# Performance work log

Hardware: AMD Instinct MI355X
Metric: run time of the kernel (lower is better)

## Reference

```python
import jax, jax.numpy as jnp
import numpy as np

D_MODEL = 1024
NUM_HEADS = 16
D_K = D_MODEL // NUM_HEADS


def setup_inputs() -> dict:
    key = jax.random.key(0)
    ks = jax.random.split(key, 9)
    s = 1.0 / np.sqrt(D_MODEL)
    x = jax.random.normal(ks[0], (2, 2048, D_MODEL), dtype=jnp.float32)
    mk = lambda k: jax.random.uniform(k, (D_MODEL, D_MODEL), jnp.float32, -s, s)
    mb = lambda k: jax.random.uniform(k, (D_MODEL,), jnp.float32, -s, s)
    return {
        "x": x,
        "Wq": mk(ks[1]), "bq": mb(ks[2]),
        "Wk": mk(ks[3]), "bk": mb(ks[4]),
        "Wv": mk(ks[5]), "bv": mb(ks[6]),
        "Wo": mk(ks[7]), "bo": mb(ks[8]),
    }


def _attn(x, Wq, bq, Wk, bk, Wv, bv, Wo, bo):
    B, S, _ = x.shape
    # torch Linear: y = x @ W.T + b; weights stored [out, in]
    def proj(W, b):
        y = jnp.einsum('bsd,ed->bse', x, W) + b
        return y.reshape(B, S, NUM_HEADS, D_K).transpose(0, 2, 1, 3)  # [B,H,S,Dk]
    Q = proj(Wq, bq)
    K = proj(Wk, bk)
    V = proj(Wv, bv)
    scale = 1.0 / np.sqrt(D_K).astype(np.float32)
    scores = jnp.einsum('bhqd,bhkd->bhqk', Q, K) * scale  # [B,H,S,S]
    # FAITHFUL to source: softmax over dim=1 (the HEAD axis), a quirk of the original code
    attn = jax.nn.softmax(scores, axis=1)
    context = jnp.einsum('bhqk,bhkd->bhqd', attn, V)  # [B,H,S,Dk]
    context = context.transpose(0, 2, 1, 3).reshape(B, S, D_MODEL)
    return jnp.einsum('bsd,ed->bse', context, Wo) + bo


def reference(x, Wq, bq, Wk, bk, Wv, bv, Wo, bo):
    return _attn(x, Wq, bq, Wk, bk, Wv, bv, Wo, bo)
```

## Files before the change

kernel.cpp:

```cpp
#include <hip/hip_runtime.h>


#define D_MODEL 1024
#define NH 16
#define DKH 64
#define SEQ 2048
#define NB 2
#define NTOK (NB * SEQ)

typedef float f32x4 __attribute__((ext_vector_type(4)));
typedef short bf16x8 __attribute__((ext_vector_type(8)));

static __device__ __forceinline__ unsigned short f2bf(float x) {
    union { float f; unsigned int u; } c; c.f = x;
    unsigned int r = (c.u + 0x7FFFu + ((c.u >> 16) & 1u)) >> 16;
    return (unsigned short)r;
}
static __device__ __forceinline__ unsigned int pack2(float a, float b) {
    return (unsigned int)f2bf(a) | ((unsigned int)f2bf(b) << 16);
}
static __device__ __forceinline__ unsigned int pack2rn(float a, float b) {
    union { float f; unsigned int u; } ca, cb; ca.f = a; cb.f = b;
    return __builtin_amdgcn_perm(cb.u + 0x8000u, ca.u + 0x8000u, 0x07060302u);
}
static __device__ __forceinline__ float bflo(unsigned int u) {
    union { unsigned int x; float f; } c; c.x = u << 16; return c.f;
}
static __device__ __forceinline__ float bfhi(unsigned int u) {
    union { unsigned int x; float f; } c; c.x = u & 0xFFFF0000u; return c.f;
}
static __device__ __forceinline__ f32x4 mfma16(uint4 a, uint4 b, f32x4 c) {
    return __builtin_amdgcn_mfma_f32_16x16x32_bf16(
        __builtin_bit_cast(bf16x8, a), __builtin_bit_cast(bf16x8, b), c, 0, 0, 0);
}
static __device__ __forceinline__ void gl_lds16(const unsigned short* g, unsigned short* l) {
    __builtin_amdgcn_global_load_lds(
        (const __attribute__((address_space(1))) unsigned int*)g,
        (__attribute__((address_space(3))) unsigned int*)l, 16, 0, 0);
}
static __device__ __forceinline__ int fsw(int row) {
    return (row & 7) ^ ((row >> 2) & 7);
}

__global__ __launch_bounds__(256) void cvt_k(const float* __restrict__ x,
                                             unsigned short* __restrict__ xb)
{
    size_t i = ((size_t)blockIdx.x * 256 + threadIdx.x) * 8;
    float4 a = *(const float4*)(x + i);
    float4 b = *(const float4*)(x + i + 4);
    uint4 p = { pack2(a.x, a.y), pack2(a.z, a.w), pack2(b.x, b.y), pack2(b.z, b.w) };
    *(uint4*)(xb + i) = p;
}

__global__ __launch_bounds__(256) void cvt_w3(
    const float* __restrict__ w0, const float* __restrict__ w1,
    const float* __restrict__ w2, unsigned short* __restrict__ outb)
{
    int sel = blockIdx.x >> 9;
    int blk = blockIdx.x & 511;
    const float* src = (sel == 0) ? w0 : (sel == 1) ? w1 : w2;
    size_t i = ((size_t)blk * 256 + threadIdx.x) * 8;
    float4 a = *(const float4*)(src + i);
    float4 b = *(const float4*)(src + i + 4);
    uint4 p = { pack2(a.x, a.y), pack2(a.z, a.w), pack2(b.x, b.y), pack2(b.z, b.w) };
    *(uint4*)(outb + (size_t)sel * D_MODEL * D_MODEL + i) = p;
}

__global__ __launch_bounds__(256) void gemm_qkv3(
    const unsigned short* __restrict__ A, const unsigned short* __restrict__ Wb3,
    const float* __restrict__ bq, const float* __restrict__ bk,
    const float* __restrict__ bv, unsigned short* __restrict__ Qh,
    unsigned short* __restrict__ Kh, unsigned short* __restrict__ Vt)
{
    __shared__ unsigned short lds[16384];
    unsigned short* lA = lds;
    unsigned short* lB = lds + 8192;
    const int tid = threadIdx.x;
    const int wv = tid >> 6, lane = tid & 63, quad = lane >> 4, lm = lane & 15;
    const int sel = blockIdx.x >> 3;
    const int m0 = blockIdx.y * 128, n0 = (blockIdx.x & 7) * 128;
    const int sub = lane >> 3, chl = (lane & 7) ^ sub;
    const unsigned short* Wb = Wb3 + (size_t)sel * D_MODEL * D_MODEL;
    const float* bias = (sel == 0) ? bq : (sel == 1) ? bk : bv;
    const float osc = (sel == 0) ? 0.125f : 1.0f;

    f32x4 acc[2][8] = {};

    for (int k0 = 0; k0 < D_MODEL; k0 += 64) {
        __syncthreads();
#pragma unroll
        for (int j = 0; j < 4; ++j) {
            int rbase = wv * 32 + j * 8;
            gl_lds16(A + (size_t)(m0 + rbase + sub) * D_MODEL + k0 + chl * 8,
                     &lA[rbase * 64]);
            gl_lds16(Wb + (size_t)(n0 + rbase + sub) * D_MODEL + k0 + chl * 8,
                     &lB[rbase * 64]);
        }
        __syncthreads();
#pragma unroll
        for (int ks = 0; ks < 2; ++ks) {
            uint4 af[2];
#pragma unroll
            for (int mt = 0; mt < 2; ++mt)
                af[mt] = *(const uint4*)&lA[(wv * 32 + mt * 16 + lm) * 64 +
                                            ((ks * 4 + quad) ^ (lm & 7)) * 8];
#pragma unroll
            for (int nt = 0; nt < 8; ++nt) {
                uint4 bf = *(const uint4*)&lB[(nt * 16 + lm) * 64 +
                                              ((ks * 4 + quad) ^ (lm & 7)) * 8];
                acc[0][nt] = mfma16(af[0], bf, acc[0][nt]);
                acc[1][nt] = mfma16(af[1], bf, acc[1][nt]);
            }
        }
    }

    if (sel < 2) {
        unsigned short* out = (sel == 0) ? Qh : Kh;
#pragma unroll
        for (int nt = 0; nt < 8; ++nt) {
            int n = n0 + nt * 16 + lm;
            float bvv = bias[n];
            int h = n >> 6, d = n & 63;
#pragma unroll
            for (int mt = 0; mt < 2; ++mt)
#pragma unroll
                for (int r = 0; r < 4; ++r) {
                    int m = m0 + wv * 32 + mt * 16 + quad * 4 + r;
                    int b = m >> 11, q = m & 2047;
                    out[((size_t)(b * NH + h) * SEQ + q) * DKH + d] =
                        f2bf((acc[mt][nt][r] + bvv) * osc);
                }
        }
    } else {
        __syncthreads();
        unsigned short* T = lds;
#pragma unroll
        for (int nt = 0; nt < 8; ++nt) {
            float bvv = bias[n0 + nt * 16 + lm];
            int nl = nt * 16 + lm;
#pragma unroll
            for (int mt = 0; mt < 2; ++mt) {
                int ml = wv * 32 + mt * 16 + quad * 4;
                uint2 p = { pack2rn(acc[mt][nt][0] + bvv, acc[mt][nt][1] + bvv),
                            pack2rn(acc[mt][nt][2] + bvv, acc[mt][nt][3] + bvv) };
                *(uint2*)&T[nl * 128 + ml] = p;
            }
        }
        __syncthreads();
        int row = tid >> 1, seg = tid & 1;
        int b = m0 >> 11, s0 = m0 & 2047;
        unsigned short* dst = Vt + ((size_t)(b * D_MODEL) + n0 + row) * SEQ + s0 + seg * 64;
        const unsigned short* src = &T[row * 128 + seg * 64];
#pragma unroll
        for (int i = 0; i < 8; ++i)
            *(uint4*)(dst + i * 8) = *(const uint4*)(src + i * 8);
    }
}

template <int KS>
__global__ __launch_bounds__(256) void psum(const unsigned short* __restrict__ OP,
                                            unsigned short* __restrict__ OPs)
{
    const size_t M = (size_t)NTOK * D_MODEL;
    size_t i = ((size_t)blockIdx.x * 256 + threadIdx.x) * 8;
    uint4 a = *(const uint4*)(OP + i);
    float lo0 = bflo(a.x), hi0 = bfhi(a.x), lo1 = bflo(a.y), hi1 = bfhi(a.y);
    float lo2 = bflo(a.z), hi2 = bfhi(a.z), lo3 = bflo(a.w), hi3 = bfhi(a.w);
#pragma unroll
    for (int p = 1; p < KS; ++p) {
        uint4 u = *(const uint4*)(OP + p * M + i);
        lo0 += bflo(u.x); hi0 += bfhi(u.x); lo1 += bflo(u.y); hi1 += bfhi(u.y);
        lo2 += bflo(u.z); hi2 += bfhi(u.z); lo3 += bflo(u.w); hi3 += bfhi(u.w);
    }
    uint4 o = { pack2(lo0, hi0), pack2(lo1, hi1), pack2(lo2, hi2), pack2(lo3, hi3) };
    *(uint4*)(OPs + i) = o;
}

__global__ __launch_bounds__(256) void gemm_osum1(
    const unsigned short* __restrict__ OPs, const unsigned short* __restrict__ WoB,
    const float* __restrict__ bias, float* __restrict__ out)
{
    __shared__ unsigned short lds[16384];
    unsigned short* lA = lds;
    unsigned short* lB = lds + 8192;
    const int tid = threadIdx.x;
    const int wv = tid >> 6, lane = tid & 63, quad = lane >> 4, lm = lane & 15;
    const int m0 = blockIdx.y * 128, n0 = blockIdx.x * 128;
    const int sub = lane >> 3, chl = (lane & 7) ^ sub;
    const int b = m0 >> 11, q0 = m0 & 2047;

    f32x4 acc[2][8] = {};

    for (int k0 = 0; k0 < D_MODEL; k0 += 64) {
        const int h = k0 >> 6;
        const unsigned short* Ab = OPs + ((size_t)(b * NH + h) * SEQ + q0) * DKH;
        __syncthreads();
#pragma unroll
        for (int j = 0; j < 4; ++j) {
            int rbase = wv * 32 + j * 8;
            gl_lds16(Ab + (size_t)(rbase + sub) * DKH + chl * 8, &lA[rbase * 64]);
            gl_lds16(WoB + (size_t)(n0 + rbase + sub) * D_MODEL + k0 + chl * 8,
                     &lB[rbase * 64]);
        }
        __syncthreads();
#pragma unroll
        for (int ks = 0; ks < 2; ++ks) {
            uint4 af[2];
#pragma unroll
            for (int mt = 0; mt < 2; ++mt)
                af[mt] = *(const uint4*)&lA[(wv * 32 + mt * 16 + lm) * 64 +
                                            ((ks * 4 + quad) ^ (lm & 7)) * 8];
#pragma unroll
            for (int nt = 0; nt < 8; ++nt) {
                uint4 bf = *(const uint4*)&lB[(nt * 16 + lm) * 64 +
                                              ((ks * 4 + quad) ^ (lm & 7)) * 8];
                acc[0][nt] = mfma16(af[0], bf, acc[0][nt]);
                acc[1][nt] = mfma16(af[1], bf, acc[1][nt]);
            }
        }
    }
#pragma unroll
    for (int nt = 0; nt < 8; ++nt) {
        int n = n0 + nt * 16 + lm;
        float bv = bias[n];
#pragma unroll
        for (int mt = 0; mt < 2; ++mt)
#pragma unroll
            for (int r = 0; r < 4; ++r) {
                int m = m0 + wv * 32 + mt * 16 + quad * 4 + r;
                out[(size_t)m * D_MODEL + n] = acc[mt][nt][r] + bv;
            }
    }
}

__global__ __launch_bounds__(256) void zker2(
    const unsigned short* __restrict__ Qh, const unsigned short* __restrict__ Kh,
    unsigned short* __restrict__ rz)
{
    __shared__ unsigned short lK[128 * 64];
    const int tid = threadIdx.x;
    const int wv = tid >> 6, lane = tid & 63, quad = lane >> 4, lm = lane & 15;
    const int q0 = blockIdx.x * 128, k0 = blockIdx.y * 128, b = blockIdx.z;
    const int srow = tid >> 3, sc = tid & 7;

    f32x4 z[2][8] = {};

    for (int h = 0; h < NH; ++h) {
        const size_t kb = ((size_t)(b * NH + h) * SEQ + k0) * DKH;
        __syncthreads();
#pragma unroll
        for (int j = 0; j < 4; ++j) {
            int row = j * 32 + srow;
            int g = sc ^ fsw(row);
            gl_lds16(Kh + kb + (size_t)row * 64 + g * 8, &lK[(j * 32 + wv * 8) * 64]);
        }
        uint4 bq[2][2];
#pragma unroll
        for (int qs = 0; qs < 2; ++qs) {
            const unsigned short* qp = Qh +
                ((size_t)(b * NH + h) * SEQ + q0 + wv * 32 + qs * 16 + lm) * DKH + quad * 8;
            bq[qs][0] = *(const uint4*)qp;
            bq[qs][1] = *(const uint4*)(qp + 32);
        }
        __syncthreads();
#pragma unroll
        for (int kt = 0; kt < 8; ++kt) {
            int krow = kt * 16 + lm;
            uint4 a0 = *(const uint4*)&lK[krow * 64 + ((quad) ^ fsw(krow)) * 8];
            uint4 a1 = *(const uint4*)&lK[krow * 64 + ((4 + quad) ^ fsw(krow)) * 8];
#pragma unroll
            for (int qs = 0; qs < 2; ++qs) {
                f32x4 sf = {0.f, 0.f, 0.f, 0.f};
                sf = mfma16(a0, bq[qs][0], sf);
                sf = mfma16(a1, bq[qs][1], sf);
#pragma unroll
                for (int r = 0; r < 4; ++r)
                    z[qs][kt][r] += __expf(sf[r]);
            }
        }
    }
#pragma unroll
    for (int qs = 0; qs < 2; ++qs) {
        int q = q0 + wv * 32 + qs * 16 + lm;
#pragma unroll
        for (int kt = 0; kt < 8; ++kt) {
            int k = k0 + kt * 16 + quad * 4;
            uint2 st = { pack2rn(1.0f / z[qs][kt][0], 1.0f / z[qs][kt][1]),
                         pack2rn(1.0f / z[qs][kt][2], 1.0f / z[qs][kt][3]) };
            *(uint2*)(rz + (size_t)(b * SEQ + q) * SEQ + k) = st;
        }
    }
}

template <int KS>
__global__ __launch_bounds__(256) void attn4(
    const unsigned short* __restrict__ Qh, const unsigned short* __restrict__ Kh,
    const unsigned short* __restrict__ Vt, const unsigned short* __restrict__ rz,
    unsigned short* __restrict__ OP)
{
    __shared__ unsigned short lK[64 * 64];
    __shared__ unsigned short lV[64 * 64];
    const int tid = threadIdx.x;
    const int wv = tid >> 6, lane = tid & 63, quad = lane >> 4, lm = lane & 15;
    const int q0 = blockIdx.x * 128;
    const int bh = blockIdx.y, b = bh >> 4, h = bh & 15;
    const int ksl = blockIdx.z;
    const int NIT = (SEQ / KS) / 64;
    const int kbeg = ksl * (SEQ / KS);
    const int q0w = q0 + wv * 32;
    const size_t hb = (size_t)(b * NH + h) * SEQ;
    const int srow = tid >> 3, sc = tid & 7;

    uint4 qf[2][2];
#pragma unroll
    for (int qs = 0; qs < 2; ++qs)
#pragma unroll
        for (int ks = 0; ks < 2; ++ks)
            qf[qs][ks] = *(const uint4*)(Qh + (hb + q0w + qs * 16 + lm) * DKH +
                                         ks * 32 + quad * 8);

    const int perm = ((lm >> 2) * 8) + (lm & 3);
    f32x4 oa[4][2] = {};

    for (int kt = 0; kt < NIT; ++kt) {
        const int kbase = kbeg + kt * 64;
        __syncthreads();
#pragma unroll
        for (int j = 0; j < 2; ++j) {
            int row = j * 32 + srow;
            int g = sc ^ fsw(row);
            gl_lds16(Kh + (hb + kbase + row) * DKH + g * 8,
                     &lK[(j * 32 + wv * 8) * 64]);
        }
#pragma unroll
        for (int j = 0; j < 2; ++j) {
            int row = j * 32 + srow;
            int g = sc ^ fsw(row);
            gl_lds16(Vt + ((size_t)(b * D_MODEL) + h * DKH + row) * SEQ + kbase + g * 8,
                     &lV[(j * 32 + wv * 8) * 64]);
        }
        uint4 rv[2][2];
#pragma unroll
        for (int qs = 0; qs < 2; ++qs)
#pragma unroll
            for (int gr = 0; gr < 2; ++gr)
                rv[gr][qs] = *(const uint4*)(rz +
                    (size_t)(b * SEQ + q0w + qs * 16 + lm) * SEQ +
                    kbase + gr * 32 + quad * 8);
        __syncthreads();

#pragma unroll
        for (int gr = 0; gr < 2; ++gr) {
            f32x4 sf[2][2] = {};
#pragma unroll
            for (int sel = 0; sel < 2; ++sel) {
                int key = gr * 32 + perm + sel * 4;
#pragma unroll
                for (int ks = 0; ks < 2; ++ks) {
                    uint4 kfv = *(const uint4*)&lK[key * 64 +
                                                   ((ks * 4 + quad) ^ fsw(key)) * 8];
                    sf[sel][0] = mfma16(kfv, qf[0][ks], sf[sel][0]);
                    sf[sel][1] = mfma16(kfv, qf[1][ks], sf[sel][1]);
                }
            }
            uint4 pk[2];
#pragma unroll
            for (int qs = 0; qs < 2; ++qs) {
                uint4 rq = rv[gr][qs];
                float p00 = __expf(sf[0][qs][0]) * bflo(rq.x);
                float p01 = __expf(sf[0][qs][1]) * bfhi(rq.x);
                float p02 = __expf(sf[0][qs][2]) * bflo(rq.y);
                float p03 = __expf(sf[0][qs][3]) * bfhi(rq.y);
                float p10 = __expf(sf[1][qs][0]) * bflo(rq.z);
                float p11 = __expf(sf[1][qs][1]) * bfhi(rq.z);
                float p12 = __expf(sf[1][qs][2]) * bflo(rq.w);
                float p13 = __expf(sf[1][qs][3]) * bfhi(rq.w);
                pk[qs].x = pack2rn(p00, p01);
                pk[qs].y = pack2rn(p02, p03);
                pk[qs].z = pack2rn(p10, p11);
                pk[qs].w = pack2rn(p12, p13);
            }
#pragma unroll
            for (int ct = 0; ct < 4; ++ct) {
                int vrow = ct * 16 + lm;
                uint4 vfv = *(const uint4*)&lV[vrow * 64 +
                                               ((gr * 4 + quad) ^ fsw(vrow)) * 8];
                oa[ct][0] = mfma16(vfv, pk[0], oa[ct][0]);
                oa[ct][1] = mfma16(vfv, pk[1], oa[ct][1]);
            }
        }
    }

    unsigned short* op = OP + (size_t)ksl * NTOK * D_MODEL;
#pragma unroll
    for (int ct = 0; ct < 4; ++ct)
#pragma unroll
        for (int qs = 0; qs < 2; ++qs) {
            uint2 st = { pack2rn(oa[ct][qs][0], oa[ct][qs][1]),
                         pack2rn(oa[ct][qs][2], oa[ct][qs][3]) };
            *(uint2*)(op + (hb + q0w + qs * 16 + lm) * DKH + ct * 16 + quad * 4) = st;
        }
}

extern "C" void kernel_launch(void* const* d_in, const int* in_sizes, int n_in,
                              void* d_out, int out_size, void* d_ws, size_t ws_size,
                              hipStream_t stream)
{
    const float* x  = (const float*)d_in[0];
    const float* Wq = (const float*)d_in[1];
    const float* bq = (const float*)d_in[2];
    const float* Wk = (const float*)d_in[3];
    const float* bk = (const float*)d_in[4];
    const float* Wv = (const float*)d_in[5];
    const float* bv = (const float*)d_in[6];
    const float* Wo = (const float*)d_in[7];
    const float* bo = (const float*)d_in[8];
    float* out = (float*)d_out;

    const size_t M  = (size_t)NTOK * D_MODEL;
    const size_t RZ = (size_t)NB * SEQ * SEQ;
    unsigned short* ws = (unsigned short*)d_ws;
    unsigned short* rzb = ws;
    unsigned short* xb  = ws;
    unsigned short* Qh  = ws + RZ;
    unsigned short* Kh  = Qh + M;
    unsigned short* Vt  = Kh + M;
    unsigned short* OP  = Vt + M;
    unsigned short* Wb3 = OP;
    unsigned short* OPs = Qh;
    unsigned short* WoB = rzb;

    const size_t need4 = (RZ + 3 * M + 4 * M) * sizeof(unsigned short);
    const size_t need2 = (RZ + 3 * M + 2 * M) * sizeof(unsigned short);
    const int KS = (ws_size >= need4) ? 4 : (ws_size >= need2) ? 2 : 1;

    cvt_k<<<2048, 256, 0, stream>>>(x, xb);
    cvt_w3<<<1536, 256, 0, stream>>>(Wq, Wk, Wv, Wb3);
    gemm_qkv3<<<dim3(24, 32), 256, 0, stream>>>(xb, Wb3, bq, bk, bv, Qh, Kh, Vt);
    zker2<<<dim3(16, 16, NB), 256, 0, stream>>>(Qh, Kh, rzb);
    if (KS == 4)      attn4<4><<<dim3(16, NB * NH, 4), 256, 0, stream>>>(Qh, Kh, Vt, rzb, OP);
    else if (KS == 2) attn4<2><<<dim3(16, NB * NH, 2), 256, 0, stream>>>(Qh, Kh, Vt, rzb, OP);
    else              attn4<1><<<dim3(16, NB * NH, 1), 256, 0, stream>>>(Qh, Kh, Vt, rzb, OP);
    cvt_k<<<512, 256, 0, stream>>>(Wo, WoB);
    if (KS == 4)      psum<4><<<2048, 256, 0, stream>>>(OP, OPs);
    else if (KS == 2) psum<2><<<2048, 256, 0, stream>>>(OP, OPs);
    else              OPs = OP;
    gemm_osum1<<<dim3(8, 32), 256, 0, stream>>>(OPs, WoB, bo, out);
}
```

Measured before the change: 276.8 us.

## Use exp2 with folded log2e scale, store log-normalizer, remap blocks per XCD

The Q projection scale now includes log2(e), so scores come out in base 2 and the hardware exp2 can be used. The per-(q,k) normalizer is stored as a negative log2 sum and fed in as the MFMA accumulator's initial value, which folds the normalization into the score and removes a multiply per element. P is packed by truncation instead of round-to-nearest. Both attention kernels also get a 1D grid with a mapping that keeps tiles sharing K/V and rz data on the same XCD for L2 locality. The costs are a bf16-rounded log normalizer and truncated P values, which lose some precision.

```diff
diff --git a/kernel.cpp b/kernel.cpp
--- a/kernel.cpp
+++ b/kernel.cpp
@@ -7,6 +7,7 @@
 #define SEQ 2048
 #define NB 2
 #define NTOK (NB * SEQ)
+#define OSC 0.180336880f
 
 typedef float f32x4 __attribute__((ext_vector_type(4)));
 typedef short bf16x8 __attribute__((ext_vector_type(8)));
@@ -22,6 +23,10 @@
 static __device__ __forceinline__ unsigned int pack2rn(float a, float b) {
     union { float f; unsigned int u; } ca, cb; ca.f = a; cb.f = b;
     return __builtin_amdgcn_perm(cb.u + 0x8000u, ca.u + 0x8000u, 0x07060302u);
+}
+static __device__ __forceinline__ unsigned int pack2tr(float a, float b) {
+    union { float f; unsigned int u; } ca, cb; ca.f = a; cb.f = b;
+    return __builtin_amdgcn_perm(cb.u, ca.u, 0x07060302u);
 }
 static __device__ __forceinline__ float bflo(unsigned int u) {
     union { unsigned int x; float f; } c; c.x = u << 16; return c.f;
@@ -82,7 +87,7 @@
     const int sub = lane >> 3, chl = (lane & 7) ^ sub;
     const unsigned short* Wb = Wb3 + (size_t)sel * D_MODEL * D_MODEL;
     const float* bias = (sel == 0) ? bq : (sel == 1) ? bk : bv;
-    const float osc = (sel == 0) ? 0.125f : 1.0f;
+    const float osc = (sel == 0) ? OSC : 1.0f;
 
     f32x4 acc[2][8] = {};
 
@@ -240,19 +245,23 @@
     __shared__ unsigned short lK[128 * 64];
     const int tid = threadIdx.x;
     const int wv = tid >> 6, lane = tid & 63, quad = lane >> 4, lm = lane & 15;
-    const int q0 = blockIdx.x * 128, k0 = blockIdx.y * 128, b = blockIdx.z;
+    const int lid = blockIdx.x;
+    const int xcd = lid & 7, slot = lid >> 3;
+    const int qb = slot & 15, col = xcd * 4 + (slot >> 4);
+    const int b = col >> 4, kb = col & 15;
+    const int q0 = qb * 128, k0 = kb * 128;
     const int srow = tid >> 3, sc = tid & 7;
 
     f32x4 z[2][8] = {};
 
     for (int h = 0; h < NH; ++h) {
-        const size_t kb = ((size_t)(b * NH + h) * SEQ + k0) * DKH;
+        const size_t kbase = ((size_t)(b * NH + h) * SEQ + k0) * DKH;
         __syncthreads();
 #pragma unroll
         for (int j = 0; j < 4; ++j) {
             int row = j * 32 + srow;
             int g = sc ^ fsw(row);
-            gl_lds16(Kh + kb + (size_t)row * 64 + g * 8, &lK[(j * 32 + wv * 8) * 64]);
+            gl_lds16(Kh + kbase + (size_t)row * 64 + g * 8, &lK[(j * 32 + wv * 8) * 64]);
         }
         uint4 bq[2][2];
 #pragma unroll
@@ -275,7 +284,7 @@
                 sf = mfma16(a1, bq[qs][1], sf);
 #pragma unroll
                 for (int r = 0; r < 4; ++r)
-                    z[qs][kt][r] += __expf(sf[r]);
+                    z[qs][kt][r] += __builtin_amdgcn_exp2f(sf[r]);
             }
         }
     }
@@ -285,8 +294,11 @@
 #pragma unroll
         for (int kt = 0; kt < 8; ++kt) {
             int k = k0 + kt * 16 + quad * 4;
-            uint2 st = { pack2rn(1.0f / z[qs][kt][0], 1.0f / z[qs][kt][1]),
-                         pack2rn(1.0f / z[qs][kt][2], 1.0f / z[qs][kt][3]) };
+            float l0 = __builtin_amdgcn_logf(z[qs][kt][0]);
+            float l1 = __builtin_amdgcn_logf(z[qs][kt][1]);
+            float l2 = __builtin_amdgcn_logf(z[qs][kt][2]);
+            float l3 = __builtin_amdgcn_logf(z[qs][kt][3]);
+            uint2 st = { pack2rn(-l0, -l1), pack2rn(-l2, -l3) };
             *(uint2*)(rz + (size_t)(b * SEQ + q) * SEQ + k) = st;
         }
     }
@@ -302,9 +314,13 @@
     __shared__ unsigned short lV[64 * 64];
     const int tid = threadIdx.x;
     const int wv = tid >> 6, lane = tid & 63, quad = lane >> 4, lm = lane & 15;
-    const int q0 = blockIdx.x * 128;
-    const int bh = blockIdx.y, b = bh >> 4, h = bh & 15;
-    const int ksl = blockIdx.z;
+    const int lid = blockIdx.x;
+    const int xcd = lid & 7, slot = lid >> 3;
+    const int qb = slot & 15;
+    const int combo = xcd * (4 * KS) + (slot >> 4);
+    const int bh = combo / KS, ksl = combo % KS;
+    const int b = bh >> 4, h = bh & 15;
+    const int q0 = qb * 128;
     const int NIT = (SEQ / KS) / 64;
     const int kbeg = ksl * (SEQ / KS);
     const int q0w = q0 + wv * 32;
@@ -351,7 +367,15 @@
 
 #pragma unroll
         for (int gr = 0; gr < 2; ++gr) {
-            f32x4 sf[2][2] = {};
+            f32x4 sf[2][2];
+#pragma unroll
+            for (int qs = 0; qs < 2; ++qs) {
+                uint4 rq = rv[gr][qs];
+                sf[0][qs][0] = bflo(rq.x); sf[0][qs][1] = bfhi(rq.x);
+                sf[0][qs][2] = bflo(rq.y); sf[0][qs][3] = bfhi(rq.y);
+                sf[1][qs][0] = bflo(rq.z); sf[1][qs][1] = bfhi(rq.z);
+                sf[1][qs][2] = bflo(rq.w); sf[1][qs][3] = bfhi(rq.w);
+            }
 #pragma unroll
             for (int sel = 0; sel < 2; ++sel) {
                 int key = gr * 32 + perm + sel * 4;
@@ -366,19 +390,18 @@
             uint4 pk[2];
 #pragma unroll
             for (int qs = 0; qs < 2; ++qs) {
-                uint4 rq = rv[gr][qs];
-                float p00 = __expf(sf[0][qs][0]) * bflo(rq.x);
-                float p01 = __expf(sf[0][qs][1]) * bfhi(rq.x);
-                float p02 = __expf(sf[0][qs][2]) * bflo(rq.y);
-                float p03 = __expf(sf[0][qs][3]) * bfhi(rq.y);
-                float p10 = __expf(sf[1][qs][0]) * bflo(rq.z);
-                float p11 = __expf(sf[1][qs][1]) * bfhi(rq.z);
-                float p12 = __expf(sf[1][qs][2]) * bflo(rq.w);
-                float p13 = __expf(sf[1][qs][3]) * bfhi(rq.w);
-                pk[qs].x = pack2rn(p00, p01);
-                pk[qs].y = pack2rn(p02, p03);
-                pk[qs].z = pack2rn(p10, p11);
-                pk[qs].w = pack2rn(p12, p13);
+                float p00 = __builtin_amdgcn_exp2f(sf[0][qs][0]);
+                float p01 = __builtin_amdgcn_exp2f(sf[0][qs][1]);
+                float p02 = __builtin_amdgcn_exp2f(sf[0][qs][2]);
+                float p03 = __builtin_amdgcn_exp2f(sf[0][qs][3]);
+                float p10 = __builtin_amdgcn_exp2f(sf[1][qs][0]);
+                float p11 = __builtin_amdgcn_exp2f(sf[1][qs][1]);
+                float p12 = __builtin_amdgcn_exp2f(sf[1][qs][2]);
+                float p13 = __builtin_amdgcn_exp2f(sf[1][qs][3]);
+                pk[qs].x = pack2tr(p00, p01);
+                pk[qs].y = pack2tr(p02, p03);
+                pk[qs].z = pack2tr(p10, p11);
+                pk[qs].w = pack2tr(p12, p13);
             }
 #pragma unroll
             for (int ct = 0; ct < 4; ++ct) {
@@ -437,10 +460,10 @@
     cvt_k<<<2048, 256, 0, stream>>>(x, xb);
     cvt_w3<<<1536, 256, 0, stream>>>(Wq, Wk, Wv, Wb3);
     gemm_qkv3<<<dim3(24, 32), 256, 0, stream>>>(xb, Wb3, bq, bk, bv, Qh, Kh, Vt);
-    zker2<<<dim3(16, 16, NB), 256, 0, stream>>>(Qh, Kh, rzb);
-    if (KS == 4)      attn4<4><<<dim3(16, NB * NH, 4), 256, 0, stream>>>(Qh, Kh, Vt, rzb, OP);
-    else if (KS == 2) attn4<2><<<dim3(16, NB * NH, 2), 256, 0, stream>>>(Qh, Kh, Vt, rzb, OP);
-    else              attn4<1><<<dim3(16, NB * NH, 1), 256, 0, stream>>>(Qh, Kh, Vt, rzb, OP);
+    zker2<<<512, 256, 0, stream>>>(Qh, Kh, rzb);
+    if (KS == 4)      attn4<4><<<2048, 256, 0, stream>>>(Qh, Kh, Vt, rzb, OP);
+    else if (KS == 2) attn4<2><<<1024, 256, 0, stream>>>(Qh, Kh, Vt, rzb, OP);
+    else              attn4<1><<<512, 256, 0, stream>>>(Qh, Kh, Vt, rzb, OP);
     cvt_k<<<512, 256, 0, stream>>>(Wo, WoB);
     if (KS == 4)      psum<4><<<2048, 256, 0, stream>>>(OP, OPs);
     else if (KS == 2) psum<2><<<2048, 256, 0, stream>>>(OP, OPs);
```

Result: faster. 268.1 us (-3.2%).
